# Kernel tuning notes

Measured on AMD Instinct MI355X. Metric: run time of the kernel, lower is better.

The kernel has to match this reference:

```python
import jax, jax.numpy as jnp
import numpy as np

IN_SIZE = 5        # per-segment features: [number, In, former_number, speed0, speed1]
HIDDEN = 128
OUT_HIDDEN = 128
OUT_SIZE = 3       # input_size = output_size + 2 (structural constraint)
T_PREDICT = 4
B, T, S = 8, 128, 128


def setup_inputs() -> dict:
    key = jax.random.key(0)
    ks = jax.random.split(key, 5)
    scale = 0.05
    return {
        "input_data": jax.random.normal(ks[0], (B, T, S, IN_SIZE), jnp.float32),
        # seg_model: fused LSTM weight over concat(x, h, h_after, h_before)
        "W_cell": jax.random.normal(ks[1], (IN_SIZE + 3 * HIDDEN, 4 * HIDDEN), jnp.float32) * scale,
        "b_cell": jnp.zeros((4 * HIDDEN,), jnp.float32),
        # FCNet layerSize=[hidden, output_hidden, output]: Linear-ReLU-Linear
        "W1": jax.random.normal(ks[2], (HIDDEN, OUT_HIDDEN), jnp.float32) * scale,
        "b1": jnp.zeros((OUT_HIDDEN,), jnp.float32),
        "W2": jax.random.normal(ks[3], (OUT_HIDDEN, OUT_SIZE), jnp.float32) * scale,
        "b2": jnp.zeros((OUT_SIZE,), jnp.float32),
    }


def _cell(x, h, c, h_after, h_before, W, b):
    # LSTM cell on concat(x, h, h_after, h_before): [B,S,IN+3H] @ [IN+3H,4H]
    z = jnp.concatenate([x, h, h_after, h_before], axis=-1) @ W + b
    i, f, g, o = jnp.split(z, 4, axis=-1)
    c_new = jax.nn.sigmoid(f) * c + jax.nn.sigmoid(i) * jnp.tanh(g)
    h_new = jax.nn.sigmoid(o) * jnp.tanh(c_new)
    return h_new, c_new


def _next_input(former_input, next_input, output):
    # faithful translation of caculate_next_input
    speed_output = output[:, 1:, 1:]                    # [B,S-1,OUT-1]
    number_output = output[:, :, 0:1]                   # [B,S,1]
    speed_input = next_input[:, 0:1, 3:]                # [B,1,IN-3]
    In = jnp.concatenate([next_input[:, 0:1, 1:2], number_output[:, :-1, :]], axis=1)
    former_number = former_input[:, :, 2:3]
    number_caculate = former_number + In - number_output
    speed_next = jnp.concatenate([speed_input, speed_output], axis=1)
    return jnp.concatenate([number_output, In, number_caculate, speed_next], axis=2)


def reference(input_data, W_cell, b_cell, W1, b1, W2, b2):
    b, t, s, f = input_data.shape
    # time-major inputs for scan: x at time k and time k+1
    x_t = jnp.transpose(input_data[:, :-1], (1, 0, 2, 3))   # [T-1,B,S,F]
    x_tp1 = jnp.transpose(input_data[:, 1:], (1, 0, 2, 3))  # [T-1,B,S,F]
    h0 = jnp.zeros((b, s, HIDDEN), input_data.dtype)
    c0 = jnp.zeros((b, s, HIDDEN), input_data.dtype)

    def step(carry, xs):
        h, c = carry
        xt, xn = xs
        # spatial neighbor shift: h_after[i] = h[i+1], h_before[i] = h[i-1]
        h_after = jnp.pad(h[:, 1:, :], ((0, 0), (0, 1), (0, 0)))
        h_before = jnp.pad(h[:, :-1, :], ((0, 0), (1, 0), (0, 0)))
        h, c = _cell(xt, h, c, h_after, h_before, W_cell, b_cell)
        out = jnp.maximum(h @ W1 + b1, 0.0) @ W2 + b2
        nd = _next_input(xt, xn, out)
        return (h, c), nd

    _, nds = jax.lax.scan(step, (h0, c0), (x_t, x_tp1))     # [T-1,B,S,F]
    # original only writes outputs for time >= t_predict
    outputs = jnp.transpose(nds[T_PREDICT:], (1, 0, 2, 3))  # [B,T-TP-1,S,F]
    return outputs
```

## Files before the change

### kernel.cpp

```cpp
#include <hip/hip_runtime.h>
#include <hip/hip_bf16.h>


#define NB 8
#define NT 128
#define NS 128
#define NSTEP 127
#define TPRED 4
#define TOUT 123

typedef __attribute__((ext_vector_type(4))) float f32x4;
typedef __attribute__((ext_vector_type(8))) short s16x8;

#define WS_WTC 0
#define WS_WT1 (512*384*2)
#define WS_HB  (WS_WT1 + 128*128*2)
#define WS_FLG (WS_HB + 2*64*2048*2)

__device__ __forceinline__ unsigned swz(unsigned off) {
    return off ^ (((off >> 8) & 7u) << 4);
}

__device__ __forceinline__ void st16_llc(void* p, unsigned v) {
    asm volatile("global_store_short %0, %1, off sc0 sc1" :: "v"(p), "v"(v) : "memory");
}
__device__ __forceinline__ void st32_llc(void* p, unsigned v) {
    asm volatile("global_store_dword %0, %1, off sc0 sc1" :: "v"(p), "v"(v) : "memory");
}
__device__ __forceinline__ unsigned ld32_llc(const void* p) {
    unsigned v;
    asm volatile("global_load_dword %0, %1, off sc0 sc1\n\ts_waitcnt vmcnt(0)"
                 : "=v"(v) : "v"(p) : "memory");
    return v;
}

__global__ void init_weights(const float* __restrict__ Wc, const float* __restrict__ W1,
                             __hip_bfloat16* __restrict__ WTc, __hip_bfloat16* __restrict__ WT1)
{
    int i = blockIdx.x * blockDim.x + threadIdx.x;
    if (i < 512*384) {
        int cpp = i / 384, k = i % 384;
        int n = cpp >> 6, rem = cpp & 63, g = rem >> 4, h = rem & 15;
        int oc = g*128 + 16*n + h;
        int row = (k < 128) ? (261 + k) : ((k < 256) ? (5 + (k - 128)) : (133 + (k - 256)));
        WTc[cpp*384 + k] = __float2bfloat16(Wc[row*512 + oc]);
    } else {
        int q = i - 512*384;
        if (q < 128*128) {
            int nn = q >> 7, k = q & 127;
            WT1[nn*128 + k] = __float2bfloat16(W1[k*128 + nn]);
        }
    }
}

__global__ __launch_bounds__(512, 2) void lstm_persist(
    const float* __restrict__ input, const float* __restrict__ Wc,
    const float* __restrict__ bc, const float* __restrict__ b1v,
    const float* __restrict__ W2, const float* __restrict__ b2,
    float* __restrict__ outp,
    const __hip_bfloat16* __restrict__ WTc, const __hip_bfloat16* __restrict__ WT1,
    unsigned short* hbu, unsigned* flags)
{
    __shared__ __align__(16) __hip_bfloat16 h_loc[130*128];
    __shared__ __align__(16) __hip_bfloat16 bl[64*136];
    __shared__ __align__(16) __hip_bfloat16 relu_l[18*128];
    __shared__ float xl[2][640];
    __shared__ float xnl[2][3];
    __shared__ float outl[17*3];
    __shared__ float w2l[3*128];
    __shared__ float b2l[3];

    const int tid  = threadIdx.x;
    const int blk  = blockIdx.x;
    const int b    = blk & 7;
    const int n    = blk >> 3;
    const int lane = tid & 63;
    const int w    = tid >> 6;
    const int arow = lane & 15;
    const int kgrp = lane >> 4;
    const int hid  = 16*n + arow;

    for (int i = tid; i < 130*128; i += 512) ((unsigned short*)h_loc)[i] = 0;
    if (tid < 384) w2l[tid] = W2[(tid & 127)*3 + (tid >> 7)];
    if (tid >= 384 && tid < 387) b2l[tid - 384] = b2[tid - 384];
    for (int i = tid; i < 64*32; i += 512) {
        int col = i >> 5, kk = i & 31;
        *(unsigned long long*)((char*)bl + col*272 + kk*8) =
            *(const unsigned long long*)((const char*)WTc + ((unsigned)(n*64 + col)*384 + 256)*2 + kk*8);
    }

    float wxr[4][5], bcr[4];
    #pragma unroll
    for (int g = 0; g < 4; ++g) {
        const int cg = g*128 + hid;
        bcr[g] = bc[cg];
        #pragma unroll
        for (int f = 0; f < 5; ++f) wxr[g][f] = Wc[f*512 + cg];
    }
    const float b1r = b1v[16*w + arow];

    s16x8 brg[4][8];
    #pragma unroll
    for (int g = 0; g < 4; ++g)
        #pragma unroll
        for (int kt = 0; kt < 8; ++kt)
            brg[g][kt] = *(const s16x8*)((const char*)WTc +
                ((unsigned)(n*64 + g*16 + arow)*384 + kt*32 + kgrp*8)*2);
    s16x8 w1r[4];
    #pragma unroll
    for (int kt = 0; kt < 4; ++kt)
        w1r[kt] = *(const s16x8*)((const char*)WT1 + ((unsigned)(16*w + arow)*128 + kt*32 + kgrp*8)*2);

    float cst[4] = {0.f, 0.f, 0.f, 0.f};
    unsigned short hregb[4] = {0, 0, 0, 0};
    unsigned* myflag = flags + b*8 + n;

    __syncthreads();

    for (int j = 0; j <= NSTEP; ++j) {
        {
            const float* xp = input + (unsigned)(b*NT + j)*640;
            xl[j&1][tid] = xp[tid];
            if (tid < 128) xl[j&1][512 + tid] = xp[512 + tid];
            if (tid >= 509 && tid < 512) { int q = tid - 509; xnl[j&1][q] = xp[(q == 0) ? 1 : (q + 2)]; }
        }
        if (j > 0) {
            if (tid < 7) {
                const int sp = tid + (tid >= n);
                const unsigned* f = flags + b*8 + sp;
                while (ld32_llc(f) < (unsigned)j)
                    __builtin_amdgcn_s_sleep(1);
            }
            __syncthreads();
            const unsigned long long* hb64 =
                (const unsigned long long*)hbu + (unsigned)((j&1)*64 + b*8)*512;
            const int s_0 = 0 + (0 >= n), s_1 = 1 + (1 >= n), s_2 = 2 + (2 >= n), s_3 = 3 + (3 >= n),
                      s_4 = 4 + (4 >= n), s_5 = 5 + (5 >= n), s_6 = 6 + (6 >= n);
            const unsigned long long *q0 = hb64 + s_0*512 + tid, *q1 = hb64 + s_1*512 + tid,
                                     *q2 = hb64 + s_2*512 + tid, *q3 = hb64 + s_3*512 + tid,
                                     *q4 = hb64 + s_4*512 + tid, *q5 = hb64 + s_5*512 + tid,
                                     *q6 = hb64 + s_6*512 + tid;
            unsigned long long g0, g1, g2, g3, g4, g5, g6;
            asm volatile(
                "global_load_dwordx2 %0, %7, off sc0 sc1\n\t"
                "global_load_dwordx2 %1, %8, off sc0 sc1\n\t"
                "global_load_dwordx2 %2, %9, off sc0 sc1\n\t"
                "global_load_dwordx2 %3, %10, off sc0 sc1\n\t"
                "global_load_dwordx2 %4, %11, off sc0 sc1\n\t"
                "global_load_dwordx2 %5, %12, off sc0 sc1\n\t"
                "global_load_dwordx2 %6, %13, off sc0 sc1\n\t"
                "s_waitcnt vmcnt(0)"
                : "=&v"(g0), "=&v"(g1), "=&v"(g2), "=&v"(g3), "=&v"(g4), "=&v"(g5), "=&v"(g6)
                : "v"(q0), "v"(q1), "v"(q2), "v"(q3), "v"(q4), "v"(q5), "v"(q6)
                : "memory");
            __builtin_amdgcn_sched_barrier(0);
            const unsigned rb = (unsigned)(((tid >> 2) + 1)*256);
            const unsigned cb = (unsigned)(4*(tid & 3))*2u;
            *(unsigned long long*)((char*)h_loc + swz(rb + 32u*s_0 + cb)) = g0;
            *(unsigned long long*)((char*)h_loc + swz(rb + 32u*s_1 + cb)) = g1;
            *(unsigned long long*)((char*)h_loc + swz(rb + 32u*s_2 + cb)) = g2;
            *(unsigned long long*)((char*)h_loc + swz(rb + 32u*s_3 + cb)) = g3;
            *(unsigned long long*)((char*)h_loc + swz(rb + 32u*s_4 + cb)) = g4;
            *(unsigned long long*)((char*)h_loc + swz(rb + 32u*s_5 + cb)) = g5;
            *(unsigned long long*)((char*)h_loc + swz(rb + 32u*s_6 + cb)) = g6;
            #pragma unroll
            for (int r = 0; r < 4; ++r)
                *(unsigned short*)((char*)h_loc +
                    swz((unsigned)((16*w + kgrp*4 + r + 1)*256 + hid*2))) = hregb[r];
        }
        __syncthreads();

        if (j < NSTEP) {
            f32x4 a0 = {0.f,0.f,0.f,0.f}, a1 = a0, a2 = a0, a3 = a0;
            const unsigned abase = (unsigned)((16*w + arow)*256 + kgrp*16);
            #pragma unroll
            for (int kt = 0; kt < 8; ++kt) {
                const s16x8 av = *(const s16x8*)((const char*)h_loc + swz(abase + kt*64));
                a0 = __builtin_amdgcn_mfma_f32_16x16x32_bf16(av, brg[0][kt], a0, 0, 0, 0);
                a1 = __builtin_amdgcn_mfma_f32_16x16x32_bf16(av, brg[1][kt], a1, 0, 0, 0);
                a2 = __builtin_amdgcn_mfma_f32_16x16x32_bf16(av, brg[2][kt], a2, 0, 0, 0);
                a3 = __builtin_amdgcn_mfma_f32_16x16x32_bf16(av, brg[3][kt], a3, 0, 0, 0);
            }
            #pragma unroll
            for (int kt = 8; kt < 12; ++kt) {
                const s16x8 av = *(const s16x8*)((const char*)h_loc + swz(abase + kt*64));
                const char* blb = (const char*)bl + (kt - 8)*64 + kgrp*16;
                a0 = __builtin_amdgcn_mfma_f32_16x16x32_bf16(av, *(const s16x8*)(blb + (arow      )*272), a0, 0, 0, 0);
                a1 = __builtin_amdgcn_mfma_f32_16x16x32_bf16(av, *(const s16x8*)(blb + (16 + arow )*272), a1, 0, 0, 0);
                a2 = __builtin_amdgcn_mfma_f32_16x16x32_bf16(av, *(const s16x8*)(blb + (32 + arow )*272), a2, 0, 0, 0);
                a3 = __builtin_amdgcn_mfma_f32_16x16x32_bf16(av, *(const s16x8*)(blb + (48 + arow )*272), a3, 0, 0, 0);
            }
            unsigned short* pub = hbu + (unsigned)(((j+1)&1)*64 + b*8 + n)*2048;
            #pragma unroll
            for (int r = 0; r < 4; ++r) {
                const int row = 16*w + kgrp*4 + r;
                const float xv0 = xl[j&1][row*5+0], xv1 = xl[j&1][row*5+1], xv2 = xl[j&1][row*5+2],
                            xv3 = xl[j&1][row*5+3], xv4 = xl[j&1][row*5+4];
                const float iv = a0[r] + bcr[0] + xv0*wxr[0][0] + xv1*wxr[0][1] + xv2*wxr[0][2] + xv3*wxr[0][3] + xv4*wxr[0][4];
                const float fv = a1[r] + bcr[1] + xv0*wxr[1][0] + xv1*wxr[1][1] + xv2*wxr[1][2] + xv3*wxr[1][3] + xv4*wxr[1][4];
                const float gv = a2[r] + bcr[2] + xv0*wxr[2][0] + xv1*wxr[2][1] + xv2*wxr[2][2] + xv3*wxr[2][3] + xv4*wxr[2][4];
                const float ov = a3[r] + bcr[3] + xv0*wxr[3][0] + xv1*wxr[3][1] + xv2*wxr[3][2] + xv3*wxr[3][3] + xv4*wxr[3][4];
                const float si = __builtin_amdgcn_rcpf(1.f + __expf(-iv));
                const float sf = __builtin_amdgcn_rcpf(1.f + __expf(-fv));
                const float so = __builtin_amdgcn_rcpf(1.f + __expf(-ov));
                const float tg = 1.f - 2.f*__builtin_amdgcn_rcpf(__expf(2.f*gv) + 1.f);
                const float cn = sf*cst[r] + si*tg;
                cst[r] = cn;
                const float tc = 1.f - 2.f*__builtin_amdgcn_rcpf(__expf(2.f*cn) + 1.f);
                const float hn = so*tc;
                __hip_bfloat16 hbv = __float2bfloat16(hn);
                unsigned short hbits = *(unsigned short*)&hbv;
                hregb[r] = hbits;
                st16_llc(pub + row*16 + arow, (unsigned)hbits);
            }
            asm volatile("s_waitcnt vmcnt(0)" ::: "memory");
            __syncthreads();
            if (tid == 0)
                st32_llc(myflag, (unsigned)(j + 1));
        }

        if (j >= TPRED + 1) {
            f32x4 c0 = {0.f,0.f,0.f,0.f}, c1 = c0;
            const unsigned w1a = (unsigned)((16*n + arow)*256 + kgrp*16);
            #pragma unroll
            for (int kt = 0; kt < 4; ++kt) {
                const s16x8 av0 = *(const s16x8*)((const char*)h_loc + swz(w1a + kt*64));
                const s16x8 av1 = *(const s16x8*)((const char*)h_loc + swz(w1a + 256 + kt*64));
                c0 = __builtin_amdgcn_mfma_f32_16x16x32_bf16(av0, w1r[kt], c0, 0, 0, 0);
                c1 = __builtin_amdgcn_mfma_f32_16x16x32_bf16(av1, w1r[kt], c1, 0, 0, 0);
            }
            #pragma unroll
            for (int r = 0; r < 4; ++r) {
                const int lr = kgrp*4 + r;
                const float v0 = fmaxf(c0[r] + b1r, 0.f);
                *(__hip_bfloat16*)((char*)relu_l + swz((unsigned)(lr*256 + (16*w + arow)*2))) = __float2bfloat16(v0);
                if (lr == 15) {
                    const float v1 = fmaxf(c1[r] + b1r, 0.f);
                    *(__hip_bfloat16*)((char*)relu_l + swz((unsigned)(16*256 + (16*w + arow)*2))) = __float2bfloat16(v1);
                }
            }
            __syncthreads();
            if (tid < 51) {
                const int m = tid / 3, p = tid - m*3;
                float s = b2l[p];
                #pragma unroll
                for (int kc = 0; kc < 16; ++kc) {
                    union { s16x8 v; unsigned short u[8]; } uu;
                    uu.v = *(const s16x8*)((const char*)relu_l + swz((unsigned)(m*256 + kc*16)));
                    #pragma unroll
                    for (int e = 0; e < 8; ++e)
                        s += __uint_as_float((unsigned)uu.u[e] << 16) * w2l[p*128 + kc*8 + e];
                }
                outl[m*3 + p] = s;
            }
            __syncthreads();
            if (tid < 16) {
                const int m = tid, grow = 16*n + m;
                const float no = outl[(m + 1)*3 + 0];
                float In, sp0, sp1;
                if (m == 0 && n == 0) { In = xnl[j&1][0]; sp0 = xnl[j&1][1]; sp1 = xnl[j&1][2]; }
                else { In = outl[m*3 + 0]; sp0 = outl[(m + 1)*3 + 1]; sp1 = outl[(m + 1)*3 + 2]; }
                const float former = xl[(j - 1)&1][grow*5 + 2];
                const long base = ((long)(b*TOUT + (j - 1 - TPRED))*NS + grow)*5;
                outp[base + 0] = no;
                outp[base + 1] = In;
                outp[base + 2] = former + In - no;
                outp[base + 3] = sp0;
                outp[base + 4] = sp1;
            }
        }
        __syncthreads();
    }
}

extern "C" void kernel_launch(void* const* d_in, const int* in_sizes, int n_in,
                              void* d_out, int out_size, void* d_ws, size_t ws_size,
                              hipStream_t stream) {
    const float* input = (const float*)d_in[0];
    const float* Wc    = (const float*)d_in[1];
    const float* bc    = (const float*)d_in[2];
    const float* W1    = (const float*)d_in[3];
    const float* b1    = (const float*)d_in[4];
    const float* W2    = (const float*)d_in[5];
    const float* b2    = (const float*)d_in[6];
    float* outp = (float*)d_out;
    char* ws = (char*)d_ws;

    __hip_bfloat16* WTc = (__hip_bfloat16*)(ws + WS_WTC);
    __hip_bfloat16* WT1 = (__hip_bfloat16*)(ws + WS_WT1);
    unsigned short* hb  = (unsigned short*)(ws + WS_HB);
    unsigned*       flg = (unsigned*)(ws + WS_FLG);

    hipMemsetAsync(ws + WS_FLG, 0, 64*4, stream);
    init_weights<<<832, 256, 0, stream>>>(Wc, W1, WTc, WT1);
    lstm_persist<<<64, 512, 0, stream>>>(input, Wc, bc, b1, W2, b2, outp, WTc, WT1, hb, flg);
}
```

Before: 950.7 us.

## Probe cross-block coherence at runtime and use L2-scoped sync when safe

At startup, each block of a batch group runs a ping-pong handshake with a neighbour using loads and stores with only sc0 set, which bypass the CU cache but not the device-wide coherence point. If all eight blocks in the group complete the handshake, they appear to share an L2/XCD, and the per-step flag polling, hidden-state publishes and neighbour loads switch from sc0 sc1 to sc0 only. The aim is lower latency on the inter-block exchange that happens every timestep. The cost is a startup barrier and handshake. It also relies on a heuristic: if the handshake passes while the blocks do not actually share a cache, results could be wrong.

```diff
diff --git a/kernel.cpp b/kernel.cpp
--- a/kernel.cpp
+++ b/kernel.cpp
@@ -16,22 +16,76 @@
 #define WS_WT1 (512*384*2)
 #define WS_HB  (WS_WT1 + 128*128*2)
 #define WS_FLG (WS_HB + 2*64*2048*2)
+#define WS_VRD (WS_FLG + 64*4)
+#define WS_BAR (WS_VRD + 64*4)
+#define WS_PING (WS_BAR + 64*4)
+#define WS_PONG (WS_PING + 64*8*4)
+#define WS_ZERO_BYTES (64*4*3 + 64*8*4*2)
 
 __device__ __forceinline__ unsigned swz(unsigned off) {
     return off ^ (((off >> 8) & 7u) << 4);
 }
 
-__device__ __forceinline__ void st16_llc(void* p, unsigned v) {
-    asm volatile("global_store_short %0, %1, off sc0 sc1" :: "v"(p), "v"(v) : "memory");
-}
-__device__ __forceinline__ void st32_llc(void* p, unsigned v) {
-    asm volatile("global_store_dword %0, %1, off sc0 sc1" :: "v"(p), "v"(v) : "memory");
-}
-__device__ __forceinline__ unsigned ld32_llc(const void* p) {
+template<bool LLC>
+__device__ __forceinline__ void st16_coh(void* p, unsigned v) {
+    if constexpr (LLC)
+        asm volatile("global_store_short %0, %1, off sc0 sc1" :: "v"(p), "v"(v) : "memory");
+    else
+        asm volatile("global_store_short %0, %1, off sc0" :: "v"(p), "v"(v) : "memory");
+}
+template<bool LLC>
+__device__ __forceinline__ void st32_coh(void* p, unsigned v) {
+    if constexpr (LLC)
+        asm volatile("global_store_dword %0, %1, off sc0 sc1" :: "v"(p), "v"(v) : "memory");
+    else
+        asm volatile("global_store_dword %0, %1, off sc0" :: "v"(p), "v"(v) : "memory");
+}
+template<bool LLC>
+__device__ __forceinline__ unsigned ld32_coh(const void* p) {
     unsigned v;
-    asm volatile("global_load_dword %0, %1, off sc0 sc1\n\ts_waitcnt vmcnt(0)"
-                 : "=v"(v) : "v"(p) : "memory");
+    if constexpr (LLC)
+        asm volatile("global_load_dword %0, %1, off sc0 sc1\n\ts_waitcnt vmcnt(0)"
+                     : "=v"(v) : "v"(p) : "memory");
+    else
+        asm volatile("global_load_dword %0, %1, off sc0\n\ts_waitcnt vmcnt(0)"
+                     : "=v"(v) : "v"(p) : "memory");
     return v;
+}
+template<bool LLC>
+__device__ __forceinline__ void ld7_coh(
+    const unsigned long long* q0, const unsigned long long* q1, const unsigned long long* q2,
+    const unsigned long long* q3, const unsigned long long* q4, const unsigned long long* q5,
+    const unsigned long long* q6,
+    unsigned long long& g0, unsigned long long& g1, unsigned long long& g2,
+    unsigned long long& g3, unsigned long long& g4, unsigned long long& g5,
+    unsigned long long& g6)
+{
+    if constexpr (LLC)
+        asm volatile(
+            "global_load_dwordx2 %0, %7, off sc0 sc1\n\t"
+            "global_load_dwordx2 %1, %8, off sc0 sc1\n\t"
+            "global_load_dwordx2 %2, %9, off sc0 sc1\n\t"
+            "global_load_dwordx2 %3, %10, off sc0 sc1\n\t"
+            "global_load_dwordx2 %4, %11, off sc0 sc1\n\t"
+            "global_load_dwordx2 %5, %12, off sc0 sc1\n\t"
+            "global_load_dwordx2 %6, %13, off sc0 sc1\n\t"
+            "s_waitcnt vmcnt(0)"
+            : "=&v"(g0), "=&v"(g1), "=&v"(g2), "=&v"(g3), "=&v"(g4), "=&v"(g5), "=&v"(g6)
+            : "v"(q0), "v"(q1), "v"(q2), "v"(q3), "v"(q4), "v"(q5), "v"(q6)
+            : "memory");
+    else
+        asm volatile(
+            "global_load_dwordx2 %0, %7, off sc0\n\t"
+            "global_load_dwordx2 %1, %8, off sc0\n\t"
+            "global_load_dwordx2 %2, %9, off sc0\n\t"
+            "global_load_dwordx2 %3, %10, off sc0\n\t"
+            "global_load_dwordx2 %4, %11, off sc0\n\t"
+            "global_load_dwordx2 %5, %12, off sc0\n\t"
+            "global_load_dwordx2 %6, %13, off sc0\n\t"
+            "s_waitcnt vmcnt(0)"
+            : "=&v"(g0), "=&v"(g1), "=&v"(g2), "=&v"(g3), "=&v"(g4), "=&v"(g5), "=&v"(g6)
+            : "v"(q0), "v"(q1), "v"(q2), "v"(q3), "v"(q4), "v"(q5), "v"(q6)
+            : "memory");
 }
 
 __global__ void init_weights(const float* __restrict__ Wc, const float* __restrict__ W1,
@@ -59,7 +113,8 @@
     const float* __restrict__ W2, const float* __restrict__ b2,
     float* __restrict__ outp,
     const __hip_bfloat16* __restrict__ WTc, const __hip_bfloat16* __restrict__ WT1,
-    unsigned short* hbu, unsigned* flags)
+    unsigned short* hbu, unsigned* flags, unsigned* vrd, unsigned* barf,
+    unsigned* pingb, unsigned* pongb)
 {
     __shared__ __align__(16) __hip_bfloat16 h_loc[130*128];
     __shared__ __align__(16) __hip_bfloat16 bl[64*136];
@@ -69,6 +124,7 @@
     __shared__ float outl[17*3];
     __shared__ float w2l[3*128];
     __shared__ float b2l[3];
+    __shared__ int s_same;
 
     const int tid  = threadIdx.x;
     const int blk  = blockIdx.x;
@@ -87,6 +143,37 @@
         int col = i >> 5, kk = i & 31;
         *(unsigned long long*)((char*)bl + col*272 + kk*8) =
             *(const unsigned long long*)((const char*)WTc + ((unsigned)(n*64 + col)*384 + 256)*2 + kk*8);
+    }
+
+    if (tid == 0) {
+        st32_coh<true>(barf + blk, 1u);
+        for (int k = 0; k < 8; ++k)
+            while (ld32_coh<true>(barf + k*8 + b) == 0u) __builtin_amdgcn_s_sleep(1);
+        const int lblk = ((n + 7) & 7)*8 + b;
+        unsigned* myping = pingb + blk*8;
+        unsigned* mypong = pongb + blk*8;
+        unsigned* inping = pingb + lblk*8;
+        unsigned* inpong = pongb + lblk*8;
+        int r_out = 0, r_in = 0;
+        st32_coh<false>(myping + 0, 1u);
+        for (int it = 0; it < 5000 && (r_out < 8 || r_in < 8); ++it) {
+            if (r_in < 8 && ld32_coh<false>(inping + r_in) == (unsigned)(r_in + 1)) {
+                st32_coh<false>(inpong + r_in, (unsigned)(r_in + 1)); ++r_in;
+            }
+            if (r_out < 8 && ld32_coh<false>(mypong + r_out) == (unsigned)(r_out + 1)) {
+                ++r_out;
+                if (r_out < 8) st32_coh<false>(myping + r_out, (unsigned)(r_out + 1));
+            }
+        }
+        st32_coh<true>(vrd + blk, (r_out == 8) ? 2u : 1u);
+        int all2 = 1;
+        for (int k = 0; k < 8; ++k) {
+            unsigned v;
+            do { v = ld32_coh<true>(vrd + k*8 + b);
+                 if (v == 0u) __builtin_amdgcn_s_sleep(1); } while (v == 0u);
+            if (v != 2u) all2 = 0;
+        }
+        s_same = all2;
     }
 
     float wxr[4][5], bcr[4];
@@ -116,6 +203,7 @@
     unsigned* myflag = flags + b*8 + n;
 
     __syncthreads();
+    const bool samex = (s_same != 0);
 
     for (int j = 0; j <= NSTEP; ++j) {
         {
@@ -128,8 +216,11 @@
             if (tid < 7) {
                 const int sp = tid + (tid >= n);
                 const unsigned* f = flags + b*8 + sp;
-                while (ld32_llc(f) < (unsigned)j)
-                    __builtin_amdgcn_s_sleep(1);
+                if (samex) {
+                    while (ld32_coh<false>(f) < (unsigned)j) __builtin_amdgcn_s_sleep(1);
+                } else {
+                    while (ld32_coh<true >(f) < (unsigned)j) __builtin_amdgcn_s_sleep(1);
+                }
             }
             __syncthreads();
             const unsigned long long* hb64 =
@@ -141,18 +232,8 @@
                                      *q4 = hb64 + s_4*512 + tid, *q5 = hb64 + s_5*512 + tid,
                                      *q6 = hb64 + s_6*512 + tid;
             unsigned long long g0, g1, g2, g3, g4, g5, g6;
-            asm volatile(
-                "global_load_dwordx2 %0, %7, off sc0 sc1\n\t"
-                "global_load_dwordx2 %1, %8, off sc0 sc1\n\t"
-                "global_load_dwordx2 %2, %9, off sc0 sc1\n\t"
-                "global_load_dwordx2 %3, %10, off sc0 sc1\n\t"
-                "global_load_dwordx2 %4, %11, off sc0 sc1\n\t"
-                "global_load_dwordx2 %5, %12, off sc0 sc1\n\t"
-                "global_load_dwordx2 %6, %13, off sc0 sc1\n\t"
-                "s_waitcnt vmcnt(0)"
-                : "=&v"(g0), "=&v"(g1), "=&v"(g2), "=&v"(g3), "=&v"(g4), "=&v"(g5), "=&v"(g6)
-                : "v"(q0), "v"(q1), "v"(q2), "v"(q3), "v"(q4), "v"(q5), "v"(q6)
-                : "memory");
+            if (samex) ld7_coh<false>(q0, q1, q2, q3, q4, q5, q6, g0, g1, g2, g3, g4, g5, g6);
+            else       ld7_coh<true >(q0, q1, q2, q3, q4, q5, q6, g0, g1, g2, g3, g4, g5, g6);
             __builtin_amdgcn_sched_barrier(0);
             const unsigned rb = (unsigned)(((tid >> 2) + 1)*256);
             const unsigned cb = (unsigned)(4*(tid & 3))*2u;
@@ -211,12 +292,15 @@
                 __hip_bfloat16 hbv = __float2bfloat16(hn);
                 unsigned short hbits = *(unsigned short*)&hbv;
                 hregb[r] = hbits;
-                st16_llc(pub + row*16 + arow, (unsigned)hbits);
+                if (samex) st16_coh<false>(pub + row*16 + arow, (unsigned)hbits);
+                else       st16_coh<true >(pub + row*16 + arow, (unsigned)hbits);
             }
             asm volatile("s_waitcnt vmcnt(0)" ::: "memory");
             __syncthreads();
-            if (tid == 0)
-                st32_llc(myflag, (unsigned)(j + 1));
+            if (tid == 0) {
+                if (samex) st32_coh<false>(myflag, (unsigned)(j + 1));
+                else       st32_coh<true >(myflag, (unsigned)(j + 1));
+            }
         }
 
         if (j >= TPRED + 1) {
@@ -290,8 +374,13 @@
     __hip_bfloat16* WT1 = (__hip_bfloat16*)(ws + WS_WT1);
     unsigned short* hb  = (unsigned short*)(ws + WS_HB);
     unsigned*       flg = (unsigned*)(ws + WS_FLG);
-
-    hipMemsetAsync(ws + WS_FLG, 0, 64*4, stream);
+    unsigned*       vrd = (unsigned*)(ws + WS_VRD);
+    unsigned*       bar = (unsigned*)(ws + WS_BAR);
+    unsigned*       png = (unsigned*)(ws + WS_PING);
+    unsigned*       pog = (unsigned*)(ws + WS_PONG);
+
+    hipMemsetAsync(ws + WS_FLG, 0, WS_ZERO_BYTES, stream);
     init_weights<<<832, 256, 0, stream>>>(Wc, W1, WTc, WT1);
-    lstm_persist<<<64, 512, 0, stream>>>(input, Wc, bc, b1, W2, b2, outp, WTc, WT1, hb, flg);
-}
+    lstm_persist<<<64, 512, 0, stream>>>(input, Wc, bc, b1, W2, b2, outp,
+                                         WTc, WT1, hb, flg, vrd, bar, png, pog);
+}
```

Result: slower. 1.972 ms (+107.4%).
